# Performance work log

Hardware: AMD Instinct MI355X
Metric: run time of the kernel (lower is better)

## Reference

```python
import jax, jax.numpy as jnp
import numpy as np

T, B, I, H = 512, 64, 128, 1024


def setup_inputs() -> dict:
    key = jax.random.key(0)
    k1, k2, k3, k4 = jax.random.split(key, 4)
    # scale recurrent weights to keep tanh in a reasonable regime (spectral-radius-ish)
    return {
        "x": jax.random.normal(k1, (T, B, I), dtype=jnp.float32),
        "h0": jnp.zeros((B, H), dtype=jnp.float32),
        "w_ih": jax.random.normal(k2, (H, I), dtype=jnp.float32) / np.sqrt(I),
        "w_hh": jax.random.normal(k3, (H, H), dtype=jnp.float32) * (0.9 / np.sqrt(H)),
        "b": jax.random.normal(k4, (H,), dtype=jnp.float32) * 0.1,
    }


def reference(x, h0, w_ih, w_hh, b):
    # ESNLayer: python loop over time -> lax.scan with the recurrent carry.
    # cell: h_t = tanh(x_t @ W_ih^T + h_{t-1} @ W_hh^T + b); out_t = h_t
    def step(h, x_t):
        h_new = jnp.tanh(x_t @ w_ih.T + h @ w_hh.T + b)  # [B, H]
        return h_new, h_new

    h_final, outputs = jax.lax.scan(step, h0, x)  # outputs: [T, B, H]
    return outputs, h_final
```

## Files before the change

kernel.cpp:

```cpp
#include <hip/hip_runtime.h>
#include <math.h>


#define T_STEPS 512
#define BATCH   64
#define HDIM    1024
#define IDIM    128
#define KDIM    1152
#define NWG     256
#define NB      4
#define POISON  0x7F7F7F7Fu

typedef float f32x4_t __attribute__((ext_vector_type(4)));

__device__ __forceinline__ void sc_load2x4(const float* p0, const float* p1,
                                           float4& a, float4& b) {
    asm volatile(
        "global_load_dwordx4 %0, %2, off sc0 sc1\n\t"
        "global_load_dwordx4 %1, %3, off sc0 sc1\n\t"
        "s_waitcnt vmcnt(0)"
        : "=&v"(a), "=&v"(b)
        : "v"(p0), "v"(p1)
        : "memory");
}

__device__ __forceinline__ void sc_store4_nodrain(float* p, float4 v) {
    f32x4_t t;
    t.x = v.x; t.y = v.y; t.z = v.z; t.w = v.w;
    asm volatile("global_store_dwordx4 %0, %1, off sc0 sc1"
                 :: "v"(p), "v"(t) : "memory");
}

__device__ __forceinline__ unsigned chk4(float4 v) {
    return (unsigned)((__float_as_uint(v.x) == POISON) |
                      (__float_as_uint(v.y) == POISON) |
                      (__float_as_uint(v.z) == POISON) |
                      (__float_as_uint(v.w) == POISON));
}

__global__ void transpose_f32(const float* __restrict__ src, float* __restrict__ dst,
                              int R, int C) {
    __shared__ float tile[64][65];
    const int tcol = threadIdx.x & 63;
    const int trow = threadIdx.x >> 6;
    const int nbx = C >> 6;
    const int bx = blockIdx.x % nbx;
    const int by = blockIdx.x / nbx;
    const int c0 = bx << 6, r0 = by << 6;
    for (int i = trow; i < 64; i += 4)
        tile[i][tcol] = src[(size_t)(r0 + i) * C + c0 + tcol];
    __syncthreads();
    for (int i = trow; i < 64; i += 4)
        dst[(size_t)(c0 + i) * R + r0 + tcol] = tile[tcol][i];
}

__global__ __launch_bounds__(512) void esn_persistent(
    const float* __restrict__ x,
    const float* __restrict__ h0,
    const float* __restrict__ WT,
    const float* __restrict__ bias,
    float* __restrict__ out,
    float* __restrict__ hfin)
{
    const int tid  = threadIdx.x;
    const int wg   = blockIdx.x;
    const int wave = tid >> 6;
    const int lane = tid & 63;
    const int jq   = lane & 7;
    const int ksub = lane >> 3;
    const int jblk = ((wg & 7) << 2) | ((wg >> 3) & 3);
    const int bgrp = wg >> 5;
    const int b0   = bgrp << 3;
    const int j0   = (jblk << 5) + (jq << 2);
    const int krec = wave << 7;
    const int kx   = HDIM + (wave << 4) + (ksub << 1);

    __shared__ float  htA[8 * 512];
    __shared__ float  htB[8 * 512];
    __shared__ float  hxA[8 * 64];
    __shared__ float  hxB[8 * 64];
    __shared__ float4 redA[8 * 8 * 5];
    __shared__ float4 redB[8 * 8 * 5];

    float4 Wv[18];
    {
        const float* wp = WT + (size_t)krec * HDIM + j0;
        #pragma unroll
        for (int i = 0; i < 4; ++i) {
            const int kk = ((i << 3) + ksub) << 2;
            const float* wk = wp + (size_t)kk * HDIM;
            Wv[i * 4 + 0] = *(const float4*)(wk);
            Wv[i * 4 + 1] = *(const float4*)(wk + HDIM);
            Wv[i * 4 + 2] = *(const float4*)(wk + 2 * HDIM);
            Wv[i * 4 + 3] = *(const float4*)(wk + 3 * HDIM);
        }
        const float* wkx = WT + (size_t)kx * HDIM + j0;
        Wv[16] = *(const float4*)(wkx);
        Wv[17] = *(const float4*)(wkx + HDIM);
    }

    float4 b4 = make_float4(0.f, 0.f, 0.f, 0.f);
    int jj = 0;
    if (lane < 8) {
        jj = (jblk << 5) + (lane << 2);
        b4 = *(const float4*)(bias + jj);
    }

    const int sbb = lane >> 5;
    const int sko = (lane & 31) << 2;
    float* hdA = htA + (wave << 9) + (sbb << 7) + sko;
    float* hdB = htB + (wave << 9) + (sbb << 7) + sko;
    const int xr = lane >> 4;
    const int xco = lane & 15;
    float* xdA = hxA + (wave << 6) + (xr << 4) + xco;
    float* xdB = hxB + (wave << 6) + (xr << 4) + xco;
    const float* hbA = htA + (wave << 9);
    const float* hbB = htB + (wave << 9);
    const float* xbA = hxA + (wave << 6);
    const float* xbB = hxB + (wave << 6);

    float xvA = x[(size_t)(b0 + xr) * IDIM + (wave << 4) + xco];
    float xvB = x[(size_t)(b0 + 4 + xr) * IDIM + (wave << 4) + xco];

    for (int t = 0; t < T_STEPS; ++t) {
        *xdA = xvA;
        if (t == 0) {
            const float* p = h0 + (size_t)(b0 + sbb) * HDIM + krec + sko;
            *(float4*)(hdA)       = *(const float4*)(p);
            *(float4*)(hdA + 256) = *(const float4*)(p + 2 * HDIM);
        } else {
            const float* p = out + ((size_t)(t - 1) * BATCH + b0 + sbb) * HDIM
                             + krec + sko;
            float4 a, b;
            do { sc_load2x4(p, p + 2 * HDIM, a, b); }
            while (__any((int)(chk4(a) | chk4(b))));
            *(float4*)(hdA)       = a;
            *(float4*)(hdA + 256) = b;
        }
        if (t + 1 < T_STEPS)
            xvA = x[((size_t)(t + 1) * BATCH + b0 + xr) * IDIM + (wave << 4) + xco];

        {
            float4 acc[NB];
            #pragma unroll
            for (int bb = 0; bb < NB; ++bb) acc[bb] = make_float4(0.f, 0.f, 0.f, 0.f);
            #pragma unroll
            for (int i = 0; i < 4; ++i) {
                const int ko = ((i << 3) + ksub) << 2;
                const float4 w0 = Wv[i * 4 + 0], w1 = Wv[i * 4 + 1];
                const float4 w2 = Wv[i * 4 + 2], w3 = Wv[i * 4 + 3];
                #pragma unroll
                for (int bb = 0; bb < NB; ++bb) {
                    float4 h4 = *(const float4*)(hbA + (bb << 7) + ko);
                    acc[bb].x = fmaf(w0.x, h4.x, acc[bb].x);
                    acc[bb].y = fmaf(w0.y, h4.x, acc[bb].y);
                    acc[bb].z = fmaf(w0.z, h4.x, acc[bb].z);
                    acc[bb].w = fmaf(w0.w, h4.x, acc[bb].w);
                    acc[bb].x = fmaf(w1.x, h4.y, acc[bb].x);
                    acc[bb].y = fmaf(w1.y, h4.y, acc[bb].y);
                    acc[bb].z = fmaf(w1.z, h4.y, acc[bb].z);
                    acc[bb].w = fmaf(w1.w, h4.y, acc[bb].w);
                    acc[bb].x = fmaf(w2.x, h4.z, acc[bb].x);
                    acc[bb].y = fmaf(w2.y, h4.z, acc[bb].y);
                    acc[bb].z = fmaf(w2.z, h4.z, acc[bb].z);
                    acc[bb].w = fmaf(w2.w, h4.z, acc[bb].w);
                    acc[bb].x = fmaf(w3.x, h4.w, acc[bb].x);
                    acc[bb].y = fmaf(w3.y, h4.w, acc[bb].y);
                    acc[bb].z = fmaf(w3.z, h4.w, acc[bb].z);
                    acc[bb].w = fmaf(w3.w, h4.w, acc[bb].w);
                }
            }
            #pragma unroll
            for (int bb = 0; bb < NB; ++bb) {
                float2 hx = *(const float2*)(xbA + (bb << 4) + (ksub << 1));
                acc[bb].x = fmaf(Wv[16].x, hx.x, acc[bb].x);
                acc[bb].y = fmaf(Wv[16].y, hx.x, acc[bb].y);
                acc[bb].z = fmaf(Wv[16].z, hx.x, acc[bb].z);
                acc[bb].w = fmaf(Wv[16].w, hx.x, acc[bb].w);
                acc[bb].x = fmaf(Wv[17].x, hx.y, acc[bb].x);
                acc[bb].y = fmaf(Wv[17].y, hx.y, acc[bb].y);
                acc[bb].z = fmaf(Wv[17].z, hx.y, acc[bb].z);
                acc[bb].w = fmaf(Wv[17].w, hx.y, acc[bb].w);
            }
            #pragma unroll
            for (int bb = 0; bb < NB; ++bb) {
                acc[bb].x += __shfl_xor(acc[bb].x, 8);
                acc[bb].y += __shfl_xor(acc[bb].y, 8);
                acc[bb].z += __shfl_xor(acc[bb].z, 8);
                acc[bb].w += __shfl_xor(acc[bb].w, 8);
                acc[bb].x += __shfl_xor(acc[bb].x, 16);
                acc[bb].y += __shfl_xor(acc[bb].y, 16);
                acc[bb].z += __shfl_xor(acc[bb].z, 16);
                acc[bb].w += __shfl_xor(acc[bb].w, 16);
                acc[bb].x += __shfl_xor(acc[bb].x, 32);
                acc[bb].y += __shfl_xor(acc[bb].y, 32);
                acc[bb].z += __shfl_xor(acc[bb].z, 32);
                acc[bb].w += __shfl_xor(acc[bb].w, 32);
            }
            if (ksub == 0) {
                #pragma unroll
                for (int bb = 0; bb < NB; ++bb)
                    redA[((wave << 3) + jq) * 5 + bb] = acc[bb];
            }
        }
        __syncthreads();
        if (wave < 4 && lane < 8) {
            float4 s = make_float4(0.f, 0.f, 0.f, 0.f);
            #pragma unroll
            for (int w = 0; w < 8; ++w) {
                float4 r = redA[((w << 3) + lane) * 5 + wave];
                s.x += r.x; s.y += r.y; s.z += r.z; s.w += r.w;
            }
            float4 o;
            o.x = tanhf(s.x + b4.x);
            o.y = tanhf(s.y + b4.y);
            o.z = tanhf(s.z + b4.z);
            o.w = tanhf(s.w + b4.w);
            sc_store4_nodrain(out + ((size_t)t * BATCH + b0 + wave) * HDIM + jj, o);
            if (t == T_STEPS - 1)
                *(float4*)(hfin + (size_t)(b0 + wave) * HDIM + jj) = o;
        }

        *xdB = xvB;
        if (t == 0) {
            const float* p = h0 + (size_t)(b0 + 4 + sbb) * HDIM + krec + sko;
            *(float4*)(hdB)       = *(const float4*)(p);
            *(float4*)(hdB + 256) = *(const float4*)(p + 2 * HDIM);
        } else {
            const float* p = out + ((size_t)(t - 1) * BATCH + b0 + 4 + sbb) * HDIM
                             + krec + sko;
            float4 a, b;
            do { sc_load2x4(p, p + 2 * HDIM, a, b); }
            while (__any((int)(chk4(a) | chk4(b))));
            *(float4*)(hdB)       = a;
            *(float4*)(hdB + 256) = b;
        }
        if (t + 1 < T_STEPS)
            xvB = x[((size_t)(t + 1) * BATCH + b0 + 4 + xr) * IDIM
                    + (wave << 4) + xco];

        {
            float4 acc[NB];
            #pragma unroll
            for (int bb = 0; bb < NB; ++bb) acc[bb] = make_float4(0.f, 0.f, 0.f, 0.f);
            #pragma unroll
            for (int i = 0; i < 4; ++i) {
                const int ko = ((i << 3) + ksub) << 2;
                const float4 w0 = Wv[i * 4 + 0], w1 = Wv[i * 4 + 1];
                const float4 w2 = Wv[i * 4 + 2], w3 = Wv[i * 4 + 3];
                #pragma unroll
                for (int bb = 0; bb < NB; ++bb) {
                    float4 h4 = *(const float4*)(hbB + (bb << 7) + ko);
                    acc[bb].x = fmaf(w0.x, h4.x, acc[bb].x);
                    acc[bb].y = fmaf(w0.y, h4.x, acc[bb].y);
                    acc[bb].z = fmaf(w0.z, h4.x, acc[bb].z);
                    acc[bb].w = fmaf(w0.w, h4.x, acc[bb].w);
                    acc[bb].x = fmaf(w1.x, h4.y, acc[bb].x);
                    acc[bb].y = fmaf(w1.y, h4.y, acc[bb].y);
                    acc[bb].z = fmaf(w1.z, h4.y, acc[bb].z);
                    acc[bb].w = fmaf(w1.w, h4.y, acc[bb].w);
                    acc[bb].x = fmaf(w2.x, h4.z, acc[bb].x);
                    acc[bb].y = fmaf(w2.y, h4.z, acc[bb].y);
                    acc[bb].z = fmaf(w2.z, h4.z, acc[bb].z);
                    acc[bb].w = fmaf(w2.w, h4.z, acc[bb].w);
                    acc[bb].x = fmaf(w3.x, h4.w, acc[bb].x);
                    acc[bb].y = fmaf(w3.y, h4.w, acc[bb].y);
                    acc[bb].z = fmaf(w3.z, h4.w, acc[bb].z);
                    acc[bb].w = fmaf(w3.w, h4.w, acc[bb].w);
                }
            }
            #pragma unroll
            for (int bb = 0; bb < NB; ++bb) {
                float2 hx = *(const float2*)(xbB + (bb << 4) + (ksub << 1));
                acc[bb].x = fmaf(Wv[16].x, hx.x, acc[bb].x);
                acc[bb].y = fmaf(Wv[16].y, hx.x, acc[bb].y);
                acc[bb].z = fmaf(Wv[16].z, hx.x, acc[bb].z);
                acc[bb].w = fmaf(Wv[16].w, hx.x, acc[bb].w);
                acc[bb].x = fmaf(Wv[17].x, hx.y, acc[bb].x);
                acc[bb].y = fmaf(Wv[17].y, hx.y, acc[bb].y);
                acc[bb].z = fmaf(Wv[17].z, hx.y, acc[bb].z);
                acc[bb].w = fmaf(Wv[17].w, hx.y, acc[bb].w);
            }
            #pragma unroll
            for (int bb = 0; bb < NB; ++bb) {
                acc[bb].x += __shfl_xor(acc[bb].x, 8);
                acc[bb].y += __shfl_xor(acc[bb].y, 8);
                acc[bb].z += __shfl_xor(acc[bb].z, 8);
                acc[bb].w += __shfl_xor(acc[bb].w, 8);
                acc[bb].x += __shfl_xor(acc[bb].x, 16);
                acc[bb].y += __shfl_xor(acc[bb].y, 16);
                acc[bb].z += __shfl_xor(acc[bb].z, 16);
                acc[bb].w += __shfl_xor(acc[bb].w, 16);
                acc[bb].x += __shfl_xor(acc[bb].x, 32);
                acc[bb].y += __shfl_xor(acc[bb].y, 32);
                acc[bb].z += __shfl_xor(acc[bb].z, 32);
                acc[bb].w += __shfl_xor(acc[bb].w, 32);
            }
            if (ksub == 0) {
                #pragma unroll
                for (int bb = 0; bb < NB; ++bb)
                    redB[((wave << 3) + jq) * 5 + bb] = acc[bb];
            }
        }
        __syncthreads();
        if (wave < 4 && lane < 8) {
            float4 s = make_float4(0.f, 0.f, 0.f, 0.f);
            #pragma unroll
            for (int w = 0; w < 8; ++w) {
                float4 r = redB[((w << 3) + lane) * 5 + wave];
                s.x += r.x; s.y += r.y; s.z += r.z; s.w += r.w;
            }
            float4 o;
            o.x = tanhf(s.x + b4.x);
            o.y = tanhf(s.y + b4.y);
            o.z = tanhf(s.z + b4.z);
            o.w = tanhf(s.w + b4.w);
            sc_store4_nodrain(out + ((size_t)t * BATCH + b0 + 4 + wave) * HDIM + jj, o);
            if (t == T_STEPS - 1)
                *(float4*)(hfin + (size_t)(b0 + 4 + wave) * HDIM + jj) = o;
        }
    }
}

extern "C" void kernel_launch(void* const* d_in, const int* in_sizes, int n_in,
                              void* d_out, int out_size, void* d_ws, size_t ws_size,
                              hipStream_t stream) {
    const float* x    = (const float*)d_in[0];
    const float* h0   = (const float*)d_in[1];
    const float* w_ih = (const float*)d_in[2];
    const float* w_hh = (const float*)d_in[3];
    const float* bias = (const float*)d_in[4];
    float* out = (float*)d_out;

    char* ws = (char*)d_ws;
    float* WT = (float*)ws;

    (void)hipMemsetAsync(out, 0x7F,
                         (size_t)T_STEPS * BATCH * HDIM * sizeof(float), stream);
    transpose_f32<<<256, 256, 0, stream>>>(w_hh, WT, HDIM, HDIM);
    transpose_f32<<<32, 256, 0, stream>>>(w_ih, WT + (size_t)HDIM * HDIM, HDIM, IDIM);
    esn_persistent<<<NWG, 512, 0, stream>>>(x, h0, WT, bias,
                                            out, out + (size_t)T_STEPS * BATCH * HDIM);
}
```

Baseline: 2.554 ms.

## Prefetch recurrent hidden state into LDS via async global_load_lds before spin-check

Instead of spinning on coherent global loads for the previous step's hidden state, each half-batch issues an asynchronous global-to-LDS load for the other half's state ahead of time, overlapping it with the current half's compute. When the state is needed, the code waits on vmcnt, reads the LDS copy, and falls back to the coherent spin-load only if poison values are still present. This aims to hide cross-workgroup load latency in the serial recurrence. The risk is that prefetches often land before producers finish, which forces the fallback path, and the vmcnt(0) wait also drains the unrelated x loads.

```diff
diff --git a/kernel.cpp b/kernel.cpp
--- a/kernel.cpp
+++ b/kernel.cpp
@@ -12,6 +12,16 @@
 #define POISON  0x7F7F7F7Fu
 
 typedef float f32x4_t __attribute__((ext_vector_type(4)));
+typedef __attribute__((address_space(3))) void lds_void;
+typedef __attribute__((address_space(1))) const void gm_void;
+
+__device__ __forceinline__ void issue_dma16(const float* g, float* l) {
+    __builtin_amdgcn_global_load_lds((gm_void*)g, (lds_void*)l, 16, 0, 17);
+}
+
+__device__ __forceinline__ void wait_vmem0(void) {
+    asm volatile("s_waitcnt vmcnt(0)" ::: "memory");
+}
 
 __device__ __forceinline__ void sc_load2x4(const float* p0, const float* p1,
                                            float4& a, float4& b) {
@@ -129,13 +139,23 @@
             *(float4*)(hdA)       = *(const float4*)(p);
             *(float4*)(hdA + 256) = *(const float4*)(p + 2 * HDIM);
         } else {
-            const float* p = out + ((size_t)(t - 1) * BATCH + b0 + sbb) * HDIM
-                             + krec + sko;
-            float4 a, b;
-            do { sc_load2x4(p, p + 2 * HDIM, a, b); }
-            while (__any((int)(chk4(a) | chk4(b))));
-            *(float4*)(hdA)       = a;
-            *(float4*)(hdA + 256) = b;
+            wait_vmem0();
+            float4 a = *(const float4*)(hdA);
+            float4 b = *(const float4*)(hdA + 256);
+            if (__any((int)(chk4(a) | chk4(b)))) {
+                const float* p = out + ((size_t)(t - 1) * BATCH + b0 + sbb) * HDIM
+                                 + krec + sko;
+                do { sc_load2x4(p, p + 2 * HDIM, a, b); }
+                while (__any((int)(chk4(a) | chk4(b))));
+                *(float4*)(hdA)       = a;
+                *(float4*)(hdA + 256) = b;
+            }
+        }
+        if (t > 0) {
+            const float* pB = out + ((size_t)(t - 1) * BATCH + b0 + 4 + sbb) * HDIM
+                              + krec + sko;
+            issue_dma16(pB, hdB);
+            issue_dma16(pB + 2 * HDIM, hdB + 256);
         }
         if (t + 1 < T_STEPS)
             xvA = x[((size_t)(t + 1) * BATCH + b0 + xr) * IDIM + (wave << 4) + xco];
@@ -227,13 +247,23 @@
             *(float4*)(hdB)       = *(const float4*)(p);
             *(float4*)(hdB + 256) = *(const float4*)(p + 2 * HDIM);
         } else {
-            const float* p = out + ((size_t)(t - 1) * BATCH + b0 + 4 + sbb) * HDIM
-                             + krec + sko;
-            float4 a, b;
-            do { sc_load2x4(p, p + 2 * HDIM, a, b); }
-            while (__any((int)(chk4(a) | chk4(b))));
-            *(float4*)(hdB)       = a;
-            *(float4*)(hdB + 256) = b;
+            wait_vmem0();
+            float4 a = *(const float4*)(hdB);
+            float4 b = *(const float4*)(hdB + 256);
+            if (__any((int)(chk4(a) | chk4(b)))) {
+                const float* p = out + ((size_t)(t - 1) * BATCH + b0 + 4 + sbb) * HDIM
+                                 + krec + sko;
+                do { sc_load2x4(p, p + 2 * HDIM, a, b); }
+                while (__any((int)(chk4(a) | chk4(b))));
+                *(float4*)(hdB)       = a;
+                *(float4*)(hdB + 256) = b;
+            }
+        }
+        if (t + 1 < T_STEPS) {
+            const float* pA = out + ((size_t)t * BATCH + b0 + sbb) * HDIM
+                              + krec + sko;
+            issue_dma16(pA, hdA);
+            issue_dma16(pA + 2 * HDIM, hdA + 256);
         }
         if (t + 1 < T_STEPS)
             xvB = x[((size_t)(t + 1) * BATCH + b0 + 4 + xr) * IDIM
```

Result: slower. 2.823 ms (+10.5%).
